# Kernel optimization log

Hardware: AMD Instinct MI355X
Metric: run time of the kernel (lower is better)

## Reference

```python
import jax, jax.numpy as jnp
import numpy as np

B, T, I, H, O = 256, 512, 64, 512, 1


def _lstm_layer(x, Wih, Whh, bih, bhh):
    # x: [B, T, in]; Wih: [4H, in]; Whh: [4H, H]
    # Precompute input contribution for all timesteps (big GEMM, no recurrence).
    xg = jnp.einsum('bti,gi->btg', x, Wih) + bih + bhh  # [B, T, 4H]
    h0 = jnp.zeros((x.shape[0], Whh.shape[1]), x.dtype)
    c0 = jnp.zeros_like(h0)

    def step(carry, xt):
        h, c = carry
        gates = xt + h @ Whh.T  # [B, 4H]
        i, f, g, o = jnp.split(gates, 4, axis=-1)  # PyTorch gate order i,f,g,o
        i = jax.nn.sigmoid(i)
        f = jax.nn.sigmoid(f)
        g = jnp.tanh(g)
        o = jax.nn.sigmoid(o)
        c = f * c + i * g
        h = o * jnp.tanh(c)
        return (h, c), h

    _, hs = jax.lax.scan(step, (h0, c0), jnp.swapaxes(xg, 0, 1))  # [T, B, H]
    return jnp.swapaxes(hs, 0, 1)  # [B, T, H]


def setup_inputs() -> dict:
    key = jax.random.key(0)
    ks = jax.random.split(key, 12)
    s = 1.0 / np.sqrt(H)
    u = lambda k, shp: jax.random.uniform(k, shp, jnp.float32, -s, s)
    return {
        'x': jax.random.normal(ks[0], (B, T, I), jnp.float32),
        'Wih0': u(ks[1], (4 * H, I)),
        'Whh0': u(ks[2], (4 * H, H)),
        'bih0': u(ks[3], (4 * H,)),
        'bhh0': u(ks[4], (4 * H,)),
        'Wih1': u(ks[5], (4 * H, H)),
        'Whh1': u(ks[6], (4 * H, H)),
        'bih1': u(ks[7], (4 * H,)),
        'bhh1': u(ks[8], (4 * H,)),
        'Wfc': u(ks[9], (O, H)),
        'bfc': u(ks[10], (O,)),
    }


def reference(x, Wih0, Whh0, bih0, bhh0, Wih1, Whh1, bih1, bhh1, Wfc, bfc):
    h1 = _lstm_layer(x, Wih0, Whh0, bih0, bhh0)   # [B, T, H]
    h2 = _lstm_layer(h1, Wih1, Whh1, bih1, bhh1)  # [B, T, H]
    return h2[:, -1] @ Wfc.T + bfc  # [B, O]
```

## Files before the change

### kernel.cpp

```cpp
#include <hip/hip_runtime.h>

typedef unsigned short u16;
typedef unsigned long long u64;
typedef short bf16x8 __attribute__((ext_vector_type(8)));
typedef float f32x4 __attribute__((ext_vector_type(4)));

#define B_ 256
#define T_ 512
#define I_ 64
#define H_ 512
#define RING 32

#define OFF_F0    0u
#define OFF_F1    32768u
#define OFF_F2    65536u
#define OFF_F3    98304u
#define OFF_B0    131072u
#define OFF_B1    139264u
#define OFF_WIH0  147456u
#define OFF_WHH0  409600u
#define OFF_WIH1  2506752u
#define OFF_WHH1  4603904u
#define OFF_HX1   6701056u
#define OFF_H1R   7225344u
#define WS_NEEDED 15613952u

#define AQ __ATOMIC_RELAXED
#define SC __HIP_MEMORY_SCOPE_AGENT

static __device__ __forceinline__ u16 f2b(float f) {
  union { float f; unsigned u; } v; v.f = f;
  unsigned r = (v.u + 0x7FFFu + ((v.u >> 16) & 1u)) >> 16;
  return (u16)r;
}
static __device__ __forceinline__ float sigm(float x) { return 1.f / (1.f + __expf(-x)); }
static __device__ __forceinline__ float tanh_(float x) { return 1.f - 2.f / (__expf(2.f * x) + 1.f); }

static __device__ __forceinline__ void spin2(const unsigned* __restrict__ pa, unsigned tg) {
  unsigned a = __hip_atomic_load(pa, AQ, SC);
  for (;;) {
    unsigned b = __hip_atomic_load(pa, AQ, SC);
    if (!__any(a < tg)) break;
    a = __hip_atomic_load(pa, AQ, SC);
    if (!__any(b < tg)) break;
  }
}

__global__ void prep_kernel(const float* __restrict__ Wih0, const float* __restrict__ Whh0,
                            const float* __restrict__ bih0, const float* __restrict__ bhh0,
                            const float* __restrict__ Wih1, const float* __restrict__ Whh1,
                            const float* __restrict__ bih1, const float* __restrict__ bhh1,
                            const float* __restrict__ bfc, float* __restrict__ out,
                            char* __restrict__ ws) {
  unsigned* flags = (unsigned*)(ws + OFF_F0);
  float* b0 = (float*)(ws + OFF_B0);
  float* b1 = (float*)(ws + OFF_B1);
  u16* wih0b = (u16*)(ws + OFF_WIH0);
  u16* whh0b = (u16*)(ws + OFF_WHH0);
  u16* wih1b = (u16*)(ws + OFF_WIH1);
  u16* whh1b = (u16*)(ws + OFF_WHH1);

  long long i = (long long)blockIdx.x * 256 + threadIdx.x;
  if (i < 32768) { __hip_atomic_store(&flags[i], 0u, AQ, SC); return; }
  i -= 32768;
  if (i < 256) { out[i] = bfc[0]; return; }
  i -= 256;
  if (i < 2048) { b0[i] = bih0[i] + bhh0[i]; return; }
  i -= 2048;
  if (i < 2048) { b1[i] = bih1[i] + bhh1[i]; return; }
  i -= 2048;
  if (i < 131072) { wih0b[i] = f2b(Wih0[i]); return; }
  i -= 131072;
  if (i < 1048576) { whh0b[i] = f2b(Whh0[i]); return; }
  i -= 1048576;
  if (i < 1048576) { wih1b[i] = f2b(Wih1[i]); return; }
  i -= 1048576;
  if (i < 1048576) { whh1b[i] = f2b(Whh1[i]); return; }
}

template <bool IS_L0>
__device__ __forceinline__ void lstm_body(
    int bx,
    const float* __restrict__ x,
    const u16* __restrict__ Wib,
    const u16* __restrict__ Whb,
    const float* __restrict__ bias,
    unsigned* __restrict__ hx32,
    u16* __restrict__ h1ring,
    const float* __restrict__ Wfc, float* __restrict__ out,
    unsigned* __restrict__ fR,
    unsigned* __restrict__ fP,
    unsigned* __restrict__ fC,
    float* __restrict__ Gp_s)
{
  const int tid = threadIdx.x;
  const int wv = tid >> 6;
  const int lane = tid & 63;
  const int quad = lane >> 4;
  const int l15 = lane & 15;
  const int jn = bx & 31;
  const int ib = bx >> 5;

  bf16x8 Bh[4][4];
#pragma unroll
  for (int r = 0; r < 4; ++r)
#pragma unroll
    for (int nt = 0; nt < 4; ++nt)
      Bh[r][nt] = *(const bf16x8*)&Whb[(size_t)(nt * 512 + jn * 16 + l15) * 512 +
                                       (wv * 4 + r) * 32 + quad * 8];
  bf16x8 Bx[4][4];
  bf16x8 Bx0[4];
  if constexpr (IS_L0) {
    if (wv < 2) {
#pragma unroll
      for (int nt = 0; nt < 4; ++nt)
        Bx0[nt] = *(const bf16x8*)&Wib[(size_t)(nt * 512 + jn * 16 + l15) * 64 +
                                       wv * 32 + quad * 8];
    }
  } else {
#pragma unroll
    for (int r = 0; r < 4; ++r)
#pragma unroll
      for (int nt = 0; nt < 4; ++nt)
        Bx[r][nt] = *(const bf16x8*)&Wib[(size_t)(nt * 512 + jn * 16 + l15) * 512 +
                                         (wv * 4 + r) * 32 + quad * 8];
  }

  const int erow = tid >> 3;
  const int ecp = tid & 7;
  float bias2[4][2];
#pragma unroll
  for (int g = 0; g < 4; ++g) {
    bias2[g][0] = bias[g * 512 + jn * 16 + 2 * ecp];
    bias2[g][1] = bias[g * 512 + jn * 16 + 2 * ecp + 1];
  }
  float cst2[2] = {0.f, 0.f};
  const f32x4 zf = {0.f, 0.f, 0.f, 0.f};
  const unsigned lineoff = ((unsigned)ib * 32 + jn) * 32;

  const int bg = ib * 32 + erow;
  const int hg = jn * 16 + 2 * ecp;
  const unsigned stoff = (unsigned)(((hg >> 3) * 256 + bg) * 4 + (ecp & 3));

  const unsigned* pollP;
  if constexpr (IS_L0)
    pollP = (lane < 32) ? &fR[lineoff + lane] : &fC[lineoff + (lane - 32)];
  else
    pollP = (lane < 32) ? &fR[lineoff + lane] : &fP[lineoff + (lane - 32)];

  if constexpr (!IS_L0) {
    if (wv == 0) spin2(&fP[lineoff + (lane & 31)], 1u);
    __syncthreads();
  }

  for (int t = 0; t < T_; ++t) {
    f32x4 acc[2][4];
#pragma unroll
    for (int mt = 0; mt < 2; ++mt)
#pragma unroll
      for (int nt = 0; nt < 4; ++nt) acc[mt][nt] = zf;

    if constexpr (IS_L0) {
      if (wv < 2) {
        const float* xp = x + ((size_t)(ib * 32 + l15) * T_ + t) * 64 + wv * 32 + quad * 8;
        const float* xq = xp + (size_t)16 * T_ * 64;
        float4 xa = *(const float4*)xp;
        float4 xb = *(const float4*)(xp + 4);
        float4 xc = *(const float4*)xq;
        float4 xd = *(const float4*)(xq + 4);
        union { unsigned u[4]; bf16x8 v; } P0, P1;
        P0.u[0] = (unsigned)f2b(xa.x) | ((unsigned)f2b(xa.y) << 16);
        P0.u[1] = (unsigned)f2b(xa.z) | ((unsigned)f2b(xa.w) << 16);
        P0.u[2] = (unsigned)f2b(xb.x) | ((unsigned)f2b(xb.y) << 16);
        P0.u[3] = (unsigned)f2b(xb.z) | ((unsigned)f2b(xb.w) << 16);
        P1.u[0] = (unsigned)f2b(xc.x) | ((unsigned)f2b(xc.y) << 16);
        P1.u[1] = (unsigned)f2b(xc.z) | ((unsigned)f2b(xc.w) << 16);
        P1.u[2] = (unsigned)f2b(xd.x) | ((unsigned)f2b(xd.y) << 16);
        P1.u[3] = (unsigned)f2b(xd.z) | ((unsigned)f2b(xd.w) << 16);
#pragma unroll
        for (int nt = 0; nt < 4; ++nt) {
          acc[0][nt] = __builtin_amdgcn_mfma_f32_16x16x32_bf16(P0.v, Bx0[nt], acc[0][nt], 0, 0, 0);
          acc[1][nt] = __builtin_amdgcn_mfma_f32_16x16x32_bf16(P1.v, Bx0[nt], acc[1][nt], 0, 0, 0);
        }
      }
      if (t && wv == 0) {
        const unsigned tg = (lane < 32) ? (unsigned)t
                            : ((t >= RING) ? (unsigned)(t - RING + 1) : 0u);
        spin2(pollP, tg);
      }
      __syncthreads();
    } else {
      const u64* hq1 = (const u64*)h1ring + (size_t)(t & (RING - 1)) * (B_ * H_ / 4);
#pragma unroll
      for (int r = 0; r < 4; ++r) {
        int ks = wv * 4 + r;
        bf16x8 af[2];
#pragma unroll
        for (int mt = 0; mt < 2; ++mt) {
          const u64* p = hq1 + (size_t)((ks * 4 + quad) * 256 + ib * 32 + mt * 16 + l15) * 2;
          union { u64 q[2]; bf16x8 v; } u;
          u.q[0] = __hip_atomic_load(p, AQ, SC);
          u.q[1] = __hip_atomic_load(p + 1, AQ, SC);
          af[mt] = u.v;
        }
#pragma unroll
        for (int nt = 0; nt < 4; ++nt) {
          acc[0][nt] = __builtin_amdgcn_mfma_f32_16x16x32_bf16(af[0], Bx[r][nt], acc[0][nt], 0, 0, 0);
          acc[1][nt] = __builtin_amdgcn_mfma_f32_16x16x32_bf16(af[1], Bx[r][nt], acc[1][nt], 0, 0, 0);
        }
      }
      if (wv == 0) {
        unsigned tP = (unsigned)(t + 2); if (tP > (unsigned)T_) tP = (unsigned)T_;
        const unsigned tg = (lane < 32) ? (unsigned)t : tP;
        spin2(pollP, tg);
      }
      __syncthreads();
    }

    __builtin_amdgcn_s_setprio(1);

    if (t) {
      const u64* hq;
      if constexpr (IS_L0)
        hq = (const u64*)h1ring + (size_t)((t - 1) & (RING - 1)) * (B_ * H_ / 4);
      else
        hq = (const u64*)hx32 + (size_t)(t & 1) * (B_ * H_ / 4);
      bf16x8 af[4][2];
#pragma unroll
      for (int r = 0; r < 4; ++r) {
        int ks = wv * 4 + r;
#pragma unroll
        for (int mt = 0; mt < 2; ++mt) {
          const u64* p = hq + (size_t)((ks * 4 + quad) * 256 + ib * 32 + mt * 16 + l15) * 2;
          union { u64 q[2]; bf16x8 v; } u;
          u.q[0] = __hip_atomic_load(p, AQ, SC);
          u.q[1] = __hip_atomic_load(p + 1, AQ, SC);
          af[r][mt] = u.v;
        }
      }
#pragma unroll
      for (int r = 0; r < 4; ++r)
#pragma unroll
        for (int mt = 0; mt < 2; ++mt)
#pragma unroll
          for (int nt = 0; nt < 4; ++nt)
            acc[mt][nt] = __builtin_amdgcn_mfma_f32_16x16x32_bf16(af[r][mt], Bh[r][nt],
                                                                  acc[mt][nt], 0, 0, 0);
    }

#pragma unroll
    for (int mt = 0; mt < 2; ++mt)
#pragma unroll
      for (int nt = 0; nt < 4; ++nt)
        *(f32x4*)&Gp_s[(nt * 16 + l15) * 132 + wv * 32 + mt * 16 + quad * 4] = acc[mt][nt];
    __syncthreads();

    {
      float pre[4][2];
#pragma unroll
      for (int g = 0; g < 4; ++g) {
#pragma unroll
        for (int j = 0; j < 2; ++j) {
          const int c = g * 16 + 2 * ecp + j;
          float s = bias2[g][j];
#pragma unroll
          for (int w = 0; w < 4; ++w) s += Gp_s[c * 132 + w * 32 + erow];
          pre[g][j] = s;
        }
      }
      float hv[2];
#pragma unroll
      for (int j = 0; j < 2; ++j) {
        float iv = sigm(pre[0][j]);
        float fv = sigm(pre[1][j]);
        float gv = tanh_(pre[2][j]);
        float ov = sigm(pre[3][j]);
        float cn = fv * cst2[j] + iv * gv;
        cst2[j] = cn;
        hv[j] = ov * tanh_(cn);
      }
      unsigned pack = (unsigned)f2b(hv[0]) | ((unsigned)f2b(hv[1]) << 16);
      if constexpr (IS_L0) {
        unsigned* ring32 = (unsigned*)h1ring;
        __hip_atomic_store(&ring32[(size_t)(t & (RING - 1)) * (B_ * H_ / 2) + stoff],
                           pack, AQ, SC);
      } else {
        __hip_atomic_store(&hx32[(size_t)((t + 1) & 1) * (B_ * H_ / 2) + stoff], pack, AQ, SC);
        if (t == T_ - 1) {
          float part = hv[0] * Wfc[hg] + hv[1] * Wfc[hg + 1];
          part += __shfl_down(part, 4, 8);
          part += __shfl_down(part, 2, 8);
          part += __shfl_down(part, 1, 8);
          if (ecp == 0) atomicAdd(&out[bg], part);
        }
      }
    }
    __builtin_amdgcn_s_setprio(0);

    __syncthreads();
    if (wv == 0) {
      unsigned val = (unsigned)(t + 1);
      if constexpr (IS_L0) {
        if (lane < 32)
          __hip_atomic_store(&fR[((unsigned)ib * 32 + lane) * 32 + jn], val, AQ, SC);
        else
          __hip_atomic_store(&fP[((unsigned)ib * 32 + (lane - 32)) * 32 + jn], val, AQ, SC);
      } else {
        if (lane < 32)
          __hip_atomic_store(&fR[((unsigned)ib * 32 + lane) * 32 + jn], val, AQ, SC);
        else
          __hip_atomic_store(&fC[((unsigned)ib * 32 + (lane - 32)) * 32 + jn], val, AQ, SC);
      }
    }
  }
}

__global__ __launch_bounds__(256, 2) void lstm_fused(
    const float* __restrict__ x,
    const u16* __restrict__ wih0, const u16* __restrict__ whh0, const float* __restrict__ b0,
    const u16* __restrict__ wih1, const u16* __restrict__ whh1, const float* __restrict__ b1,
    unsigned* __restrict__ hx1, u16* __restrict__ h1ring,
    const float* __restrict__ Wfc, float* __restrict__ out,
    unsigned* __restrict__ f0, unsigned* __restrict__ f1, unsigned* __restrict__ f2,
    unsigned* __restrict__ f3)
{
  __shared__ __align__(16) float Gp_s[64 * 132];
  if (blockIdx.x < 256)
    lstm_body<true>(blockIdx.x, x, wih0, whh0, b0, (unsigned*)nullptr, h1ring,
                    (const float*)nullptr, (float*)nullptr, f0, f1, f3, Gp_s);
  else
    lstm_body<false>(blockIdx.x - 256, (const float*)nullptr, wih1, whh1, b1, hx1, h1ring,
                     Wfc, out, f2, f1, f3, Gp_s);
}

extern "C" void kernel_launch(void* const* d_in, const int* in_sizes, int n_in,
                              void* d_out, int out_size, void* d_ws, size_t ws_size,
                              hipStream_t stream) {
  if (ws_size < (size_t)WS_NEEDED) return;

  const float* x    = (const float*)d_in[0];
  const float* Wih0 = (const float*)d_in[1];
  const float* Whh0 = (const float*)d_in[2];
  const float* bih0 = (const float*)d_in[3];
  const float* bhh0 = (const float*)d_in[4];
  const float* Wih1 = (const float*)d_in[5];
  const float* Whh1 = (const float*)d_in[6];
  const float* bih1 = (const float*)d_in[7];
  const float* bhh1 = (const float*)d_in[8];
  const float* Wfc  = (const float*)d_in[9];
  const float* bfc  = (const float*)d_in[10];

  char* ws = (char*)d_ws;
  unsigned* f0   = (unsigned*)(ws + OFF_F0);
  unsigned* f1   = (unsigned*)(ws + OFF_F1);
  unsigned* f2   = (unsigned*)(ws + OFF_F2);
  unsigned* f3   = (unsigned*)(ws + OFF_F3);
  float* b0      = (float*)(ws + OFF_B0);
  float* b1      = (float*)(ws + OFF_B1);
  u16* wih0b     = (u16*)(ws + OFF_WIH0);
  u16* whh0b     = (u16*)(ws + OFF_WHH0);
  u16* wih1b     = (u16*)(ws + OFF_WIH1);
  u16* whh1b     = (u16*)(ws + OFF_WHH1);
  unsigned* hx1  = (unsigned*)(ws + OFF_HX1);
  u16* h1ring    = (u16*)(ws + OFF_H1R);
  float* out     = (float*)d_out;

  prep_kernel<<<12948, 256, 0, stream>>>(Wih0, Whh0, bih0, bhh0, Wih1, Whh1, bih1, bhh1,
                                         bfc, out, ws);

  lstm_fused<<<512, 256, 0, stream>>>(x, wih0b, whh0b, b0, wih1b, whh1b, b1,
                                      hx1, h1ring, Wfc, out, f0, f1, f2, f3);
}
```

Baseline: 2.497 ms.

## Replace end-of-step barrier with LDS flag handshake and double-buffer gate scratch

Drops the second __syncthreads per timestep. Wave 0 now spins on per-wave LDS done flags before publishing the global progress flags, and the gate-scratch LDS buffer is double-buffered by timestep parity so the next step's writes cannot race the current reads. The block-to-(ib,jn) mapping also changes so consecutive blocks share a column slice, not a batch slice, which changes CU/XCD placement. This cuts barrier stalls on the recurrence critical path but doubles LDS use per block, which may hurt the 2-blocks-per-CU occupancy, and the spin-wait adds risk.

```diff
diff --git a/kernel.cpp b/kernel.cpp
--- a/kernel.cpp
+++ b/kernel.cpp
@@ -80,7 +80,7 @@
 
 template <bool IS_L0>
 __device__ __forceinline__ void lstm_body(
-    int bx,
+    int ib, int jn,
     const float* __restrict__ x,
     const u16* __restrict__ Wib,
     const u16* __restrict__ Whb,
@@ -91,15 +91,14 @@
     unsigned* __restrict__ fR,
     unsigned* __restrict__ fP,
     unsigned* __restrict__ fC,
-    float* __restrict__ Gp_s)
+    float* __restrict__ Gp_s,
+    unsigned* __restrict__ done_s)
 {
   const int tid = threadIdx.x;
   const int wv = tid >> 6;
   const int lane = tid & 63;
   const int quad = lane >> 4;
   const int l15 = lane & 15;
-  const int jn = bx & 31;
-  const int ib = bx >> 5;
 
   bf16x8 Bh[4][4];
 #pragma unroll
@@ -248,11 +247,12 @@
                                                                   acc[mt][nt], 0, 0, 0);
     }
 
+    float* __restrict__ Gp = Gp_s + (t & 1) * (64 * 132);
 #pragma unroll
     for (int mt = 0; mt < 2; ++mt)
 #pragma unroll
       for (int nt = 0; nt < 4; ++nt)
-        *(f32x4*)&Gp_s[(nt * 16 + l15) * 132 + wv * 32 + mt * 16 + quad * 4] = acc[mt][nt];
+        *(f32x4*)&Gp[(nt * 16 + l15) * 132 + wv * 32 + mt * 16 + quad * 4] = acc[mt][nt];
     __syncthreads();
 
     {
@@ -264,7 +264,7 @@
           const int c = g * 16 + 2 * ecp + j;
           float s = bias2[g][j];
 #pragma unroll
-          for (int w = 0; w < 4; ++w) s += Gp_s[c * 132 + w * 32 + erow];
+          for (int w = 0; w < 4; ++w) s += Gp[c * 132 + w * 32 + erow];
           pre[g][j] = s;
         }
       }
@@ -297,9 +297,18 @@
     }
     __builtin_amdgcn_s_setprio(0);
 
-    __syncthreads();
-    if (wv == 0) {
-      unsigned val = (unsigned)(t + 1);
+    asm volatile("s_waitcnt vmcnt(0)" ::: "memory");
+    if (wv) {
+      if (lane == 0)
+        __hip_atomic_store(&done_s[wv], (unsigned)(t + 1), __ATOMIC_RELEASE,
+                           __HIP_MEMORY_SCOPE_WORKGROUP);
+    } else {
+      const int di = (lane & 3) ? (lane & 3) : 1;
+      unsigned dv;
+      do {
+        dv = __hip_atomic_load(&done_s[di], __ATOMIC_ACQUIRE, __HIP_MEMORY_SCOPE_WORKGROUP);
+      } while (__any(dv < (unsigned)(t + 1)));
+      const unsigned val = (unsigned)(t + 1);
       if constexpr (IS_L0) {
         if (lane < 32)
           __hip_atomic_store(&fR[((unsigned)ib * 32 + lane) * 32 + jn], val, AQ, SC);
@@ -324,13 +333,17 @@
     unsigned* __restrict__ f0, unsigned* __restrict__ f1, unsigned* __restrict__ f2,
     unsigned* __restrict__ f3)
 {
-  __shared__ __align__(16) float Gp_s[64 * 132];
-  if (blockIdx.x < 256)
-    lstm_body<true>(blockIdx.x, x, wih0, whh0, b0, (unsigned*)nullptr, h1ring,
-                    (const float*)nullptr, (float*)nullptr, f0, f1, f3, Gp_s);
+  __shared__ __align__(16) float Gp_s[2 * 64 * 132];
+  __shared__ unsigned done_s[4];
+  if (threadIdx.x < 4) done_s[threadIdx.x] = 0u;
+  __syncthreads();
+  const int bx = blockIdx.x;
+  if (bx < 256)
+    lstm_body<true>(bx & 7, bx >> 3, x, wih0, whh0, b0, (unsigned*)nullptr, h1ring,
+                    (const float*)nullptr, (float*)nullptr, f0, f1, f3, Gp_s, done_s);
   else
-    lstm_body<false>(blockIdx.x - 256, (const float*)nullptr, wih1, whh1, b1, hx1, h1ring,
-                     Wfc, out, f2, f1, f3, Gp_s);
+    lstm_body<false>((bx - 256) & 7, (bx - 256) >> 3, (const float*)nullptr, wih1, whh1, b1,
+                     hx1, h1ring, Wfc, out, f2, f1, f3, Gp_s, done_s);
 }
 
 extern "C" void kernel_launch(void* const* d_in, const int* in_sizes, int n_in,
```

Result: slower. 2.800 ms (+12.2%).
